# Kernel tuning notes

Hardware: AMD Instinct MI355X
Metric: run time of the kernel (lower is better)

The kernel has to match this reference:

```python
import jax, jax.numpy as jnp
import numpy as np

B, T, IN = 128, 512, 3          # batch, stroke seq len, (dx,dy,pen)
A, H = 77, 512                  # alphabet size, hidden size
KW, KM, U = 10, 20, 64          # window mixtures, MDN mixtures, char seq len
OUT = 6 * KM + 1                # MDN output size


def setup_inputs() -> dict:
    key = jax.random.key(0)
    ks = jax.random.split(key, 16)
    p = lambda k, *sh: (jax.random.normal(k, sh, jnp.float32) * 0.05)
    in1 = IN + A            # lstm1 input: [x_t, w_prev]
    in2 = IN + A + H        # lstm2 input: [x_t, w_t, h1]
    return dict(
        x=jax.random.normal(ks[0], (B, T, IN), jnp.float32),
        c_seq=jax.random.uniform(ks[1], (B, U, A), jnp.float32),
        Wih1=p(ks[2], 4 * H, in1), Whh1=p(ks[3], 4 * H, H),
        bih1=p(ks[4], 4 * H), bhh1=p(ks[5], 4 * H),
        Wih2=p(ks[6], 4 * H, in2), Whh2=p(ks[7], 4 * H, H),
        bih2=p(ks[8], 4 * H), bhh2=p(ks[9], 4 * H),
        W_abk=p(ks[10], 3 * KW, H), b_abk=p(ks[11], 3 * KW),
        W_fc2=p(ks[12], OUT, H), b_fc2=p(ks[13], OUT),
    )


def _lstm_cell(xt, h, c, Wih, Whh, bih, bhh):
    # torch gate order: i, f, g, o
    z = xt @ Wih.T + h @ Whh.T + bih + bhh
    i, f, g, o = jnp.split(z, 4, axis=-1)
    c_new = jax.nn.sigmoid(f) * c + jax.nn.sigmoid(i) * jnp.tanh(g)
    h_new = jax.nn.sigmoid(o) * jnp.tanh(c_new)
    return h_new, c_new


def reference(x, c_seq, Wih1, Whh1, bih1, bhh1, Wih2, Whh2, bih2, bhh2,
              W_abk, b_abk, W_fc2, b_fc2):
    Bsz = x.shape[0]
    u = jnp.arange(c_seq.shape[1], dtype=jnp.float32)  # [U]

    def step(carry, x_t):
        h1, c1, h2, c2, kappa, w_pre = carry
        # first LSTM on [x_t, w_{t-1}]
        h1, c1 = _lstm_cell(jnp.concatenate([x_t, w_pre], -1), h1, c1,
                            Wih1, Whh1, bih1, bhh1)
        # attention window params
        abk = h1 @ W_abk.T + b_abk
        a_hat, b_hat, k_hat = jnp.split(abk, 3, axis=-1)
        alpha, beta = jnp.exp(a_hat), jnp.exp(b_hat)
        kappa = kappa + jnp.exp(k_hat)
        # phi[b,u] = sum_k alpha * exp(-beta * (kappa - u)^2)
        phi = jnp.sum(alpha[:, None, :] *
                      jnp.exp(-beta[:, None, :] *
                              (kappa[:, None, :] - u[None, :, None]) ** 2),
                      axis=2)                      # [B, U]
        w_t = jnp.einsum('bu,bua->ba', phi, c_seq)  # [B, A]
        # second LSTM on [x_t, w_t, h1]
        h2, c2 = _lstm_cell(jnp.concatenate([x_t, w_t, h1], -1), h2, c2,
                            Wih2, Whh2, bih2, bhh2)
        out = h2 @ W_fc2.T + b_fc2                  # [B, OUT]
        return (h1, c1, h2, c2, kappa, w_t), out

    z = lambda *sh: jnp.zeros(sh, x.dtype)
    carry0 = (z(Bsz, H), z(Bsz, H), z(Bsz, H), z(Bsz, H),
              z(Bsz, KW), z(Bsz, A))
    _, outs = jax.lax.scan(step, carry0, jnp.swapaxes(x, 0, 1))
    outs = jnp.swapaxes(outs, 0, 1)                 # [B, T, OUT]

    # MixtureDensityLayer
    K = KM
    pi = jax.nn.softmax(outs[..., :K], axis=-1)
    mu1 = outs[..., K:2 * K]
    mu2 = outs[..., 2 * K:3 * K]
    std1 = jnp.exp(outs[..., 3 * K:4 * K])
    std2 = jnp.exp(outs[..., 4 * K:5 * K])
    corr = jnp.tanh(outs[..., 5 * K:6 * K])
    eot = jax.nn.sigmoid(outs[..., -1:])
    return (pi, mu1, mu2, std1, std2, corr, eot)
```

## Files before the change

kernel.cpp:

```cpp
#include <hip/hip_runtime.h>
#include <math.h>

#define BB   128
#define TT   512
#define INX  3
#define AA   77
#define HH   512
#define KWD  10
#define KMD  20
#define UU   64
#define OUTD 121
#define IN1  80
#define IN2  592

#define MT   8
#define NU   8
#define GRT  (HH/NU)
#define MTL  (BB/MT)

#define P1   84
#define P2   596
#define PH   516
#define PZ   36

#define BH   (BB*HH)
#define BA   (BB*AA)
#define BKW  (BB*KWD)

__device__ __forceinline__ float sigf(float x) { return 1.0f / (1.0f + expf(-x)); }

__device__ __forceinline__ float dot4(float4 w, float4 a) {
    return w.x * a.x + w.y * a.y + w.z * a.z + w.w * a.w;
}

__device__ __forceinline__ void fc2_post(const float* __restrict__ h2r,
                                         const float* __restrict__ W_fc2,
                                         const float* __restrict__ b_fc2,
                                         float* __restrict__ out,
                                         int brow, int tprev, int tid,
                                         float* sY, float* sRed)
{
    if (tid < OUTD) {
        const float4* wr = (const float4*)(W_fc2 + (size_t)tid * HH);
        const float4* hv = (const float4*)h2r;
        float acc = b_fc2[tid];
#pragma unroll 4
        for (int k = 0; k < HH / 4; ++k)
            acc += dot4(wr[k], hv[k]);
        sY[tid] = acc;
    }
    __syncthreads();
    if (tid == 0) {
        float mx = sY[0];
        for (int i = 1; i < KMD; ++i) mx = fmaxf(mx, sY[i]);
        float s = 0.f;
        for (int i = 0; i < KMD; ++i) s += expf(sY[i] - mx);
        sRed[0] = mx; sRed[1] = s;
    }
    __syncthreads();
    if (tid < OUTD) {
        const size_t SZ = (size_t)BB * TT * KMD;
        const size_t bt = (size_t)brow * TT + tprev;
        float y = sY[tid];
        if      (tid <     KMD) out[             bt * KMD + tid          ] = expf(y - sRed[0]) / sRed[1];
        else if (tid < 2 * KMD) out[    SZ +     bt * KMD + (tid -   KMD)] = y;
        else if (tid < 3 * KMD) out[2 * SZ +     bt * KMD + (tid - 2*KMD)] = y;
        else if (tid < 4 * KMD) out[3 * SZ +     bt * KMD + (tid - 3*KMD)] = expf(y);
        else if (tid < 5 * KMD) out[4 * SZ +     bt * KMD + (tid - 4*KMD)] = expf(y);
        else if (tid < 6 * KMD) out[5 * SZ +     bt * KMD + (tid - 5*KMD)] = tanhf(y);
        else                    out[6 * SZ + bt] = sigf(y);
    }
}

__global__ __launch_bounds__(256, 4) void k1(
    const float* __restrict__ x,
    const float* __restrict__ Wih1, const float* __restrict__ Whh1,
    const float* __restrict__ bih1, const float* __restrict__ bhh1,
    const float* __restrict__ W_fc2, const float* __restrict__ b_fc2,
    const float* __restrict__ h1_old, float* __restrict__ h1_new,
    float* __restrict__ c1,
    const float* __restrict__ w_pre, const float* __restrict__ h2_prev,
    float* __restrict__ out, int t)
{
    __shared__ float sIn[MT][P1];
    __shared__ float sH[MT][PH];
    __shared__ float sZ[MT][PZ];
    __shared__ float sY[OUTD];
    __shared__ float sRed[2];

    const int tid  = threadIdx.x;
    const int grt  = blockIdx.x;
    const int mtl  = blockIdx.y;
    const int row0 = mtl * MT, unit0 = grt * NU;

    {
        const int r = tid >> 5, c0 = tid & 31;
        const int b = row0 + r;
        for (int c = c0; c < IN1; c += 32)
            sIn[r][c] = (c < INX) ? x[((size_t)b * TT + t) * INX + c]
                                  : w_pre[(size_t)b * AA + (c - INX)];
        const float4* src = (const float4*)(h1_old + (size_t)b * HH);
        float4* dst = (float4*)&sH[r][0];
        for (int c = c0; c < HH / 4; c += 32) dst[c] = src[c];
    }
    __syncthreads();

    {
        const int m = tid & 7, s = tid >> 3;
        const int g = s >> 3, jl = s & 7;
        const int wrow = g * HH + unit0 + jl;
        float acc0 = bih1[wrow] + bhh1[wrow], acc1 = 0.f, acc2 = 0.f, acc3 = 0.f;

        const float4* wp = (const float4*)(Wih1 + (size_t)wrow * IN1);
        const float4* ap = (const float4*)&sIn[m][0];
#pragma unroll
        for (int k = 0; k < IN1 / 4; k += 4) {
            float4 w0 = wp[k], w1 = wp[k+1], w2 = wp[k+2], w3 = wp[k+3];
            float4 a0 = ap[k], a1 = ap[k+1], a2 = ap[k+2], a3 = ap[k+3];
            acc0 += dot4(w0, a0); acc1 += dot4(w1, a1);
            acc2 += dot4(w2, a2); acc3 += dot4(w3, a3);
        }
        const float4* vp = (const float4*)(Whh1 + (size_t)wrow * HH);
        const float4* hp = (const float4*)&sH[m][0];
#pragma unroll 2
        for (int k = 0; k < HH / 4; k += 4) {
            float4 w0 = vp[k], w1 = vp[k+1], w2 = vp[k+2], w3 = vp[k+3];
            float4 a0 = hp[k], a1 = hp[k+1], a2 = hp[k+2], a3 = hp[k+3];
            acc0 += dot4(w0, a0); acc1 += dot4(w1, a1);
            acc2 += dot4(w2, a2); acc3 += dot4(w3, a3);
        }
        sZ[m][s] = acc0 + acc1 + acc2 + acc3;
    }
    __syncthreads();

    if (tid < MT * NU) {
        const int m = tid & 7, jl = tid >> 3;
        const float zi = sZ[m][jl],      zf = sZ[m][8 + jl];
        const float zg = sZ[m][16 + jl], zo = sZ[m][24 + jl];
        const size_t gi = (size_t)(row0 + m) * HH + unit0 + jl;
        const float cold = c1[gi];
        const float cn = sigf(zf) * cold + sigf(zi) * tanhf(zg);
        c1[gi] = cn;
        h1_new[gi] = sigf(zo) * tanhf(cn);
    }

    if (t > 0 && grt < MT) {
        const int brow = row0 + grt;
        fc2_post(h2_prev + (size_t)brow * HH, W_fc2, b_fc2, out, brow, t - 1, tid, sY, sRed);
    }
}

__global__ __launch_bounds__(256) void k2(
    const float* __restrict__ c_seq,
    const float* __restrict__ W_abk, const float* __restrict__ b_abk,
    const float* __restrict__ h1_cur,
    const float* __restrict__ kap_old, float* __restrict__ kap_new,
    float* __restrict__ w_new)
{
    __shared__ float sH1[HH];
    __shared__ float sAbk[32];
    __shared__ float sAl[KWD], sBe[KWD], sKa[KWD];
    __shared__ float sPhi[UU];

    const int tid = threadIdx.x;
    const int b   = blockIdx.x;

    if (tid < HH / 4)
        ((float4*)sH1)[tid] = ((const float4*)(h1_cur + (size_t)b * HH))[tid];
    __syncthreads();

    {
        const int o = tid >> 3, kk = tid & 7;
        float acc = 0.f;
        if (o < 3 * KWD) {
            const float4* wp = (const float4*)(W_abk + (size_t)o * HH) + kk * 16;
            const float4* hp = (const float4*)sH1 + kk * 16;
#pragma unroll
            for (int k = 0; k < 16; ++k)
                acc += dot4(wp[k], hp[k]);
        }
        acc += __shfl_xor(acc, 1);
        acc += __shfl_xor(acc, 2);
        acc += __shfl_xor(acc, 4);
        if (o < 3 * KWD && kk == 0) sAbk[o] = acc + b_abk[o];
    }
    __syncthreads();

    if (tid < KWD) {
        const float al = expf(sAbk[tid]);
        const float be = expf(sAbk[KWD + tid]);
        const float ka = kap_old[(size_t)b * KWD + tid] + expf(sAbk[2 * KWD + tid]);
        sAl[tid] = al; sBe[tid] = be; sKa[tid] = ka;
        kap_new[(size_t)b * KWD + tid] = ka;
    }
    __syncthreads();

    if (tid < UU) {
        const float u = (float)tid;
        float s = 0.f;
#pragma unroll
        for (int k = 0; k < KWD; ++k) {
            const float d = sKa[k] - u;
            s += sAl[k] * expf(-sBe[k] * d * d);
        }
        sPhi[tid] = s;
    }
    __syncthreads();

    if (tid < AA) {
        float s = 0.f;
        const float* cp = c_seq + (size_t)b * UU * AA + tid;
#pragma unroll 4
        for (int u = 0; u < UU; ++u) s += sPhi[u] * cp[(size_t)u * AA];
        w_new[(size_t)b * AA + tid] = s;
    }
}

__global__ __launch_bounds__(256, 4) void k3(
    const float* __restrict__ x,
    const float* __restrict__ Wih2, const float* __restrict__ Whh2,
    const float* __restrict__ bih2, const float* __restrict__ bhh2,
    const float* __restrict__ h1_cur, const float* __restrict__ w_cur,
    const float* __restrict__ h2_old, float* __restrict__ h2_new,
    float* __restrict__ c2, int t)
{
    __shared__ float sIn[MT][P2];
    __shared__ float sH2[MT][PH];
    __shared__ float sZ[MT][PZ];

    const int tid  = threadIdx.x;
    const int grt  = blockIdx.x;
    const int mtl  = blockIdx.y;
    const int row0 = mtl * MT, unit0 = grt * NU;

    {
        const int r = tid >> 5, c0 = tid & 31;
        const int b = row0 + r;
        for (int c = c0; c < IN1; c += 32)
            sIn[r][c] = (c < INX) ? x[((size_t)b * TT + t) * INX + c]
                                  : w_cur[(size_t)b * AA + (c - INX)];
        const float4* s1 = (const float4*)(h1_cur + (size_t)b * HH);
        float4* d1 = (float4*)&sIn[r][IN1];
        const float4* s2 = (const float4*)(h2_old + (size_t)b * HH);
        float4* d2 = (float4*)&sH2[r][0];
        for (int c = c0; c < HH / 4; c += 32) { d1[c] = s1[c]; d2[c] = s2[c]; }
    }
    __syncthreads();

    {
        const int m = tid & 7, s = tid >> 3;
        const int g = s >> 3, jl = s & 7;
        const int wrow = g * HH + unit0 + jl;
        float acc0 = bih2[wrow] + bhh2[wrow], acc1 = 0.f, acc2 = 0.f, acc3 = 0.f;

        const float4* wp = (const float4*)(Wih2 + (size_t)wrow * IN2);
        const float4* ap = (const float4*)&sIn[m][0];
#pragma unroll 2
        for (int k = 0; k < IN2 / 4; k += 4) {
            float4 w0 = wp[k], w1 = wp[k+1], w2 = wp[k+2], w3 = wp[k+3];
            float4 a0 = ap[k], a1 = ap[k+1], a2 = ap[k+2], a3 = ap[k+3];
            acc0 += dot4(w0, a0); acc1 += dot4(w1, a1);
            acc2 += dot4(w2, a2); acc3 += dot4(w3, a3);
        }
        const float4* vp = (const float4*)(Whh2 + (size_t)wrow * HH);
        const float4* hp = (const float4*)&sH2[m][0];
#pragma unroll 2
        for (int k = 0; k < HH / 4; k += 4) {
            float4 w0 = vp[k], w1 = vp[k+1], w2 = vp[k+2], w3 = vp[k+3];
            float4 a0 = hp[k], a1 = hp[k+1], a2 = hp[k+2], a3 = hp[k+3];
            acc0 += dot4(w0, a0); acc1 += dot4(w1, a1);
            acc2 += dot4(w2, a2); acc3 += dot4(w3, a3);
        }
        sZ[m][s] = acc0 + acc1 + acc2 + acc3;
    }
    __syncthreads();

    if (tid < MT * NU) {
        const int m = tid & 7, jl = tid >> 3;
        const float zi = sZ[m][jl],      zf = sZ[m][8 + jl];
        const float zg = sZ[m][16 + jl], zo = sZ[m][24 + jl];
        const size_t gi = (size_t)(row0 + m) * HH + unit0 + jl;
        const float cold = c2[gi];
        const float cn = sigf(zf) * cold + sigf(zi) * tanhf(zg);
        c2[gi] = cn;
        h2_new[gi] = sigf(zo) * tanhf(cn);
    }
}

__global__ __launch_bounds__(128) void fc2_final(
    const float* __restrict__ h2_last,
    const float* __restrict__ W_fc2, const float* __restrict__ b_fc2,
    float* __restrict__ out)
{
    __shared__ float sY[OUTD];
    __shared__ float sRed[2];
    const int brow = blockIdx.x;
    fc2_post(h2_last + (size_t)brow * HH, W_fc2, b_fc2, out, brow, TT - 1, threadIdx.x, sY, sRed);
}

extern "C" void kernel_launch(void* const* d_in, const int* in_sizes, int n_in,
                              void* d_out, int out_size, void* d_ws, size_t ws_size,
                              hipStream_t stream) {
    const float* x     = (const float*)d_in[0];
    const float* c_seq = (const float*)d_in[1];
    const float* Wih1  = (const float*)d_in[2];
    const float* Whh1  = (const float*)d_in[3];
    const float* bih1  = (const float*)d_in[4];
    const float* bhh1  = (const float*)d_in[5];
    const float* Wih2  = (const float*)d_in[6];
    const float* Whh2  = (const float*)d_in[7];
    const float* bih2  = (const float*)d_in[8];
    const float* bhh2  = (const float*)d_in[9];
    const float* W_abk = (const float*)d_in[10];
    const float* b_abk = (const float*)d_in[11];
    const float* W_fc2 = (const float*)d_in[12];
    const float* b_fc2 = (const float*)d_in[13];
    float* out = (float*)d_out;

    float* ws  = (float*)d_ws;
    float* h1b = ws;
    float* h2b = ws + 2 * BH;
    float* c1  = ws + 4 * BH;
    float* c2  = ws + 5 * BH;
    float* kap = ws + 6 * BH;
    float* wb  = ws + 6 * BH + 2 * BKW;
    const size_t used = (size_t)6 * BH + 2 * BKW + 2 * BA;

    hipMemsetAsync(d_ws, 0, used * sizeof(float), stream);

    const dim3 grid(GRT, MTL), blk(256);
    for (int t = 0; t < TT; ++t) {
        const int p = t & 1;
        k1<<<grid, blk, 0, stream>>>(x, Wih1, Whh1, bih1, bhh1, W_fc2, b_fc2,
                                     h1b + (size_t)p * BH, h1b + (size_t)(1 - p) * BH, c1,
                                     wb + (size_t)p * BA, h2b + (size_t)p * BH, out, t);
        k2<<<dim3(BB), blk, 0, stream>>>(c_seq, W_abk, b_abk,
                                         h1b + (size_t)(1 - p) * BH,
                                         kap + (size_t)p * BKW, kap + (size_t)(1 - p) * BKW,
                                         wb + (size_t)(1 - p) * BA);
        k3<<<grid, blk, 0, stream>>>(x, Wih2, Whh2, bih2, bhh2,
                                     h1b + (size_t)(1 - p) * BH, wb + (size_t)(1 - p) * BA,
                                     h2b + (size_t)p * BH, h2b + (size_t)(1 - p) * BH, c2, t);
    }
    fc2_final<<<dim3(BB), dim3(128), 0, stream>>>(h2b, W_fc2, b_fc2, out);
}
```

Measured before the change: 48.08 ms.

## Restructure LSTM gate matvec: 4 gates per thread with split-K reduction

Each thread now computes all four gates (i,f,g,o) for one hidden unit and batch row over a quarter of the concatenated input, and the four K-partials are summed in shared memory. Inputs and hidden state are packed into one concatenated shared buffer. Blocks grow to 512 threads and 16 units each, so there are half as many blocks and each shared activation load is reused across four weight rows. The cost is a split-K reduction step, weight loads strided across four separate rows, and fewer blocks, which may lower occupancy.

After: 43.82 ms. 8.9% less time.

```diff
diff --git a/kernel.cpp b/kernel.cpp
--- a/kernel.cpp
+++ b/kernel.cpp
@@ -14,14 +14,12 @@
 #define IN2  592
 
 #define MT   8
-#define NU   8
-#define GRT  (HH/NU)
+#define NJ   16
+#define GRT  (HH/NJ)
 #define MTL  (BB/MT)
 
-#define P1   84
-#define P2   596
-#define PH   516
-#define PZ   36
+#define PC1  596
+#define PC3  1108
 
 #define BH   (BB*HH)
 #define BA   (BB*AA)
@@ -72,7 +70,7 @@
     }
 }
 
-__global__ __launch_bounds__(256, 4) void k1(
+__global__ __launch_bounds__(512, 4) void k1(
     const float* __restrict__ x,
     const float* __restrict__ Wih1, const float* __restrict__ Whh1,
     const float* __restrict__ bih1, const float* __restrict__ bhh1,
@@ -82,66 +80,80 @@
     const float* __restrict__ w_pre, const float* __restrict__ h2_prev,
     float* __restrict__ out, int t)
 {
-    __shared__ float sIn[MT][P1];
-    __shared__ float sH[MT][PH];
-    __shared__ float sZ[MT][PZ];
+    __shared__ float sCat[MT][PC1];
+    __shared__ float sZp[4][MT][68];
     __shared__ float sY[OUTD];
     __shared__ float sRed[2];
 
     const int tid  = threadIdx.x;
     const int grt  = blockIdx.x;
     const int mtl  = blockIdx.y;
-    const int row0 = mtl * MT, unit0 = grt * NU;
-
-    {
-        const int r = tid >> 5, c0 = tid & 31;
+    const int row0 = mtl * MT, unit0 = grt * NJ;
+
+    {
+        const int r = tid >> 6, c = tid & 63;
         const int b = row0 + r;
-        for (int c = c0; c < IN1; c += 32)
-            sIn[r][c] = (c < INX) ? x[((size_t)b * TT + t) * INX + c]
-                                  : w_pre[(size_t)b * AA + (c - INX)];
-        const float4* src = (const float4*)(h1_old + (size_t)b * HH);
-        float4* dst = (float4*)&sH[r][0];
-        for (int c = c0; c < HH / 4; c += 32) dst[c] = src[c];
-    }
-    __syncthreads();
-
-    {
-        const int m = tid & 7, s = tid >> 3;
-        const int g = s >> 3, jl = s & 7;
-        const int wrow = g * HH + unit0 + jl;
-        float acc0 = bih1[wrow] + bhh1[wrow], acc1 = 0.f, acc2 = 0.f, acc3 = 0.f;
-
-        const float4* wp = (const float4*)(Wih1 + (size_t)wrow * IN1);
-        const float4* ap = (const float4*)&sIn[m][0];
+        const float4* s1 = (const float4*)(h1_old + (size_t)b * HH);
+        float4* d1 = (float4*)&sCat[r][IN1];
+        for (int i = c; i < HH / 4; i += 64) d1[i] = s1[i];
+        for (int i = c; i < IN1; i += 64)
+            sCat[r][i] = (i < INX) ? x[((size_t)b * TT + t) * INX + i]
+                                   : w_pre[(size_t)b * AA + (i - INX)];
+    }
+    __syncthreads();
+
+    {
+        const int m = tid & 7, j = (tid >> 3) & 15, kq = tid >> 7;
+        const int i0 = kq * 37, i1 = i0 + 37;
+        const int u = unit0 + j;
+        float a0 = 0.f, a1 = 0.f, a2 = 0.f, a3 = 0.f;
+        const float4* sc = (const float4*)&sCat[m][0];
+
+        const float4* w0a = (const float4*)Wih1 + (size_t)u * 20;
+        const float4* w1a = (const float4*)Wih1 + (size_t)(HH + u) * 20;
+        const float4* w2a = (const float4*)Wih1 + (size_t)(2 * HH + u) * 20;
+        const float4* w3a = (const float4*)Wih1 + (size_t)(3 * HH + u) * 20;
+        const int aEnd = (i1 < 20) ? i1 : 20;
+        for (int i = i0; i < aEnd; ++i) {
+            float4 a = sc[i];
+            a0 += dot4(w0a[i], a); a1 += dot4(w1a[i], a);
+            a2 += dot4(w2a[i], a); a3 += dot4(w3a[i], a);
+        }
+        const float4* w0b = (const float4*)Whh1 + (size_t)u * 128;
+        const float4* w1b = (const float4*)Whh1 + (size_t)(HH + u) * 128;
+        const float4* w2b = (const float4*)Whh1 + (size_t)(2 * HH + u) * 128;
+        const float4* w3b = (const float4*)Whh1 + (size_t)(3 * HH + u) * 128;
+        const int bSt = (i0 > 20) ? i0 : 20;
+#pragma unroll 4
+        for (int i = bSt; i < i1; ++i) {
+            float4 a = sc[i];
+            const int k = i - 20;
+            a0 += dot4(w0b[k], a); a1 += dot4(w1b[k], a);
+            a2 += dot4(w2b[k], a); a3 += dot4(w3b[k], a);
+        }
+        sZp[kq][m][j]      = a0;
+        sZp[kq][m][16 + j] = a1;
+        sZp[kq][m][32 + j] = a2;
+        sZp[kq][m][48 + j] = a3;
+    }
+    __syncthreads();
+
+    if (tid < MT * NJ) {
+        const int m = tid >> 4, j = tid & 15;
+        const int u = unit0 + j;
+        float z[4];
 #pragma unroll
-        for (int k = 0; k < IN1 / 4; k += 4) {
-            float4 w0 = wp[k], w1 = wp[k+1], w2 = wp[k+2], w3 = wp[k+3];
-            float4 a0 = ap[k], a1 = ap[k+1], a2 = ap[k+2], a3 = ap[k+3];
-            acc0 += dot4(w0, a0); acc1 += dot4(w1, a1);
-            acc2 += dot4(w2, a2); acc3 += dot4(w3, a3);
-        }
-        const float4* vp = (const float4*)(Whh1 + (size_t)wrow * HH);
-        const float4* hp = (const float4*)&sH[m][0];
-#pragma unroll 2
-        for (int k = 0; k < HH / 4; k += 4) {
-            float4 w0 = vp[k], w1 = vp[k+1], w2 = vp[k+2], w3 = vp[k+3];
-            float4 a0 = hp[k], a1 = hp[k+1], a2 = hp[k+2], a3 = hp[k+3];
-            acc0 += dot4(w0, a0); acc1 += dot4(w1, a1);
-            acc2 += dot4(w2, a2); acc3 += dot4(w3, a3);
-        }
-        sZ[m][s] = acc0 + acc1 + acc2 + acc3;
-    }
-    __syncthreads();
-
-    if (tid < MT * NU) {
-        const int m = tid & 7, jl = tid >> 3;
-        const float zi = sZ[m][jl],      zf = sZ[m][8 + jl];
-        const float zg = sZ[m][16 + jl], zo = sZ[m][24 + jl];
-        const size_t gi = (size_t)(row0 + m) * HH + unit0 + jl;
+        for (int g = 0; g < 4; ++g) {
+            const int wr = g * HH + u;
+            z[g] = bih1[wr] + bhh1[wr]
+                 + sZp[0][m][g * 16 + j] + sZp[1][m][g * 16 + j]
+                 + sZp[2][m][g * 16 + j] + sZp[3][m][g * 16 + j];
+        }
+        const size_t gi = (size_t)(row0 + m) * HH + u;
         const float cold = c1[gi];
-        const float cn = sigf(zf) * cold + sigf(zi) * tanhf(zg);
+        const float cn = sigf(z[1]) * cold + sigf(z[0]) * tanhf(z[2]);
         c1[gi] = cn;
-        h1_new[gi] = sigf(zo) * tanhf(cn);
+        h1_new[gi] = sigf(z[3]) * tanhf(cn);
     }
 
     if (t > 0 && grt < MT) {
@@ -216,7 +228,7 @@
     }
 }
 
-__global__ __launch_bounds__(256, 4) void k3(
+__global__ __launch_bounds__(512, 4) void k3(
     const float* __restrict__ x,
     const float* __restrict__ Wih2, const float* __restrict__ Whh2,
     const float* __restrict__ bih2, const float* __restrict__ bhh2,
@@ -224,66 +236,81 @@
     const float* __restrict__ h2_old, float* __restrict__ h2_new,
     float* __restrict__ c2, int t)
 {
-    __shared__ float sIn[MT][P2];
-    __shared__ float sH2[MT][PH];
-    __shared__ float sZ[MT][PZ];
+    __shared__ float sCat[MT][PC3];
+    __shared__ float sZp[4][MT][68];
 
     const int tid  = threadIdx.x;
     const int grt  = blockIdx.x;
     const int mtl  = blockIdx.y;
-    const int row0 = mtl * MT, unit0 = grt * NU;
-
-    {
-        const int r = tid >> 5, c0 = tid & 31;
+    const int row0 = mtl * MT, unit0 = grt * NJ;
+
+    {
+        const int r = tid >> 6, c = tid & 63;
         const int b = row0 + r;
-        for (int c = c0; c < IN1; c += 32)
-            sIn[r][c] = (c < INX) ? x[((size_t)b * TT + t) * INX + c]
-                                  : w_cur[(size_t)b * AA + (c - INX)];
         const float4* s1 = (const float4*)(h1_cur + (size_t)b * HH);
-        float4* d1 = (float4*)&sIn[r][IN1];
         const float4* s2 = (const float4*)(h2_old + (size_t)b * HH);
-        float4* d2 = (float4*)&sH2[r][0];
-        for (int c = c0; c < HH / 4; c += 32) { d1[c] = s1[c]; d2[c] = s2[c]; }
-    }
-    __syncthreads();
-
-    {
-        const int m = tid & 7, s = tid >> 3;
-        const int g = s >> 3, jl = s & 7;
-        const int wrow = g * HH + unit0 + jl;
-        float acc0 = bih2[wrow] + bhh2[wrow], acc1 = 0.f, acc2 = 0.f, acc3 = 0.f;
-
-        const float4* wp = (const float4*)(Wih2 + (size_t)wrow * IN2);
-        const float4* ap = (const float4*)&sIn[m][0];
-#pragma unroll 2
-        for (int k = 0; k < IN2 / 4; k += 4) {
-            float4 w0 = wp[k], w1 = wp[k+1], w2 = wp[k+2], w3 = wp[k+3];
-            float4 a0 = ap[k], a1 = ap[k+1], a2 = ap[k+2], a3 = ap[k+3];
-            acc0 += dot4(w0, a0); acc1 += dot4(w1, a1);
-            acc2 += dot4(w2, a2); acc3 += dot4(w3, a3);
-        }
-        const float4* vp = (const float4*)(Whh2 + (size_t)wrow * HH);
-        const float4* hp = (const float4*)&sH2[m][0];
-#pragma unroll 2
-        for (int k = 0; k < HH / 4; k += 4) {
-            float4 w0 = vp[k], w1 = vp[k+1], w2 = vp[k+2], w3 = vp[k+3];
-            float4 a0 = hp[k], a1 = hp[k+1], a2 = hp[k+2], a3 = hp[k+3];
-            acc0 += dot4(w0, a0); acc1 += dot4(w1, a1);
-            acc2 += dot4(w2, a2); acc3 += dot4(w3, a3);
-        }
-        sZ[m][s] = acc0 + acc1 + acc2 + acc3;
-    }
-    __syncthreads();
-
-    if (tid < MT * NU) {
-        const int m = tid & 7, jl = tid >> 3;
-        const float zi = sZ[m][jl],      zf = sZ[m][8 + jl];
-        const float zg = sZ[m][16 + jl], zo = sZ[m][24 + jl];
-        const size_t gi = (size_t)(row0 + m) * HH + unit0 + jl;
+        float4* d1 = (float4*)&sCat[r][IN1];
+        float4* d2 = (float4*)&sCat[r][IN2];
+        for (int i = c; i < HH / 4; i += 64) { d1[i] = s1[i]; d2[i] = s2[i]; }
+        for (int i = c; i < IN1; i += 64)
+            sCat[r][i] = (i < INX) ? x[((size_t)b * TT + t) * INX + i]
+                                   : w_cur[(size_t)b * AA + (i - INX)];
+    }
+    __syncthreads();
+
+    {
+        const int m = tid & 7, j = (tid >> 3) & 15, kq = tid >> 7;
+        const int i0 = kq * 69, i1 = i0 + 69;
+        const int u = unit0 + j;
+        float a0 = 0.f, a1 = 0.f, a2 = 0.f, a3 = 0.f;
+        const float4* sc = (const float4*)&sCat[m][0];
+
+        const float4* w0a = (const float4*)Wih2 + (size_t)u * 148;
+        const float4* w1a = (const float4*)Wih2 + (size_t)(HH + u) * 148;
+        const float4* w2a = (const float4*)Wih2 + (size_t)(2 * HH + u) * 148;
+        const float4* w3a = (const float4*)Wih2 + (size_t)(3 * HH + u) * 148;
+        const int aEnd = (i1 < 148) ? i1 : 148;
+#pragma unroll 4
+        for (int i = i0; i < aEnd; ++i) {
+            float4 a = sc[i];
+            a0 += dot4(w0a[i], a); a1 += dot4(w1a[i], a);
+            a2 += dot4(w2a[i], a); a3 += dot4(w3a[i], a);
+        }
+        const float4* w0b = (const float4*)Whh2 + (size_t)u * 128;
+        const float4* w1b = (const float4*)Whh2 + (size_t)(HH + u) * 128;
+        const float4* w2b = (const float4*)Whh2 + (size_t)(2 * HH + u) * 128;
+        const float4* w3b = (const float4*)Whh2 + (size_t)(3 * HH + u) * 128;
+        const int bSt = (i0 > 148) ? i0 : 148;
+#pragma unroll 4
+        for (int i = bSt; i < i1; ++i) {
+            float4 a = sc[i];
+            const int k = i - 148;
+            a0 += dot4(w0b[k], a); a1 += dot4(w1b[k], a);
+            a2 += dot4(w2b[k], a); a3 += dot4(w3b[k], a);
+        }
+        sZp[kq][m][j]      = a0;
+        sZp[kq][m][16 + j] = a1;
+        sZp[kq][m][32 + j] = a2;
+        sZp[kq][m][48 + j] = a3;
+    }
+    __syncthreads();
+
+    if (tid < MT * NJ) {
+        const int m = tid >> 4, j = tid & 15;
+        const int u = unit0 + j;
+        float z[4];
+#pragma unroll
+        for (int g = 0; g < 4; ++g) {
+            const int wr = g * HH + u;
+            z[g] = bih2[wr] + bhh2[wr]
+                 + sZp[0][m][g * 16 + j] + sZp[1][m][g * 16 + j]
+                 + sZp[2][m][g * 16 + j] + sZp[3][m][g * 16 + j];
+        }
+        const size_t gi = (size_t)(row0 + m) * HH + u;
         const float cold = c2[gi];
-        const float cn = sigf(zf) * cold + sigf(zi) * tanhf(zg);
+        const float cn = sigf(z[1]) * cold + sigf(z[0]) * tanhf(z[2]);
         c2[gi] = cn;
-        h2_new[gi] = sigf(zo) * tanhf(cn);
+        h2_new[gi] = sigf(z[3]) * tanhf(cn);
     }
 }
 
@@ -328,16 +355,16 @@
 
     hipMemsetAsync(d_ws, 0, used * sizeof(float), stream);
 
-    const dim3 grid(GRT, MTL), blk(256);
+    const dim3 grid(GRT, MTL), blk(512);
     for (int t = 0; t < TT; ++t) {
         const int p = t & 1;
         k1<<<grid, blk, 0, stream>>>(x, Wih1, Whh1, bih1, bhh1, W_fc2, b_fc2,
                                      h1b + (size_t)p * BH, h1b + (size_t)(1 - p) * BH, c1,
                                      wb + (size_t)p * BA, h2b + (size_t)p * BH, out, t);
-        k2<<<dim3(BB), blk, 0, stream>>>(c_seq, W_abk, b_abk,
-                                         h1b + (size_t)(1 - p) * BH,
-                                         kap + (size_t)p * BKW, kap + (size_t)(1 - p) * BKW,
-                                         wb + (size_t)(1 - p) * BA);
+        k2<<<dim3(BB), dim3(256), 0, stream>>>(c_seq, W_abk, b_abk,
+                                               h1b + (size_t)(1 - p) * BH,
+                                               kap + (size_t)p * BKW, kap + (size_t)(1 - p) * BKW,
+                                               wb + (size_t)(1 - p) * BA);
         k3<<<grid, blk, 0, stream>>>(x, Wih2, Whh2, bih2, bhh2,
                                      h1b + (size_t)(1 - p) * BH, wb + (size_t)(1 - p) * BA,
                                      h2b + (size_t)p * BH, h2b + (size_t)(1 - p) * BH, c2, t);
```
